# Kernel tuning notes

Hardware: AMD Instinct MI355X
Metric: run time of the kernel (lower is better)

The kernel has to match this reference:

```python
import jax, jax.numpy as jnp
import numpy as np
from jax import lax


def setup_inputs() -> dict:
    key = jax.random.key(0)
    kx, kw = jax.random.split(key)
    x = jax.random.normal(kx, (32, 3, 8192), dtype=jnp.float32)
    weight = jax.random.normal(kw, (128, 3, 64), dtype=jnp.float32)
    return {"x": x, "weight": weight}


def reference(x, weight):
    # x: [B, C, L], weight: [O, C, K]
    K = weight.shape[2]
    # Cross-correlation (conv1d, no bias, valid padding): [B, O, L-K+1]
    conv_out = lax.conv_general_dilated(
        x, weight, window_strides=(1,), padding='VALID',
        dimension_numbers=('NCH', 'OIH', 'NCH'))
    # Half squared norm of each shapelet: [O]
    w_norm = jnp.sum(weight ** 2, axis=(1, 2)) / 2
    # Half squared norm of each length-K window, via cumulative sums
    # (avoids materializing the [B, C, W, K] unfold tensor)
    sq = jnp.sum(x ** 2, axis=1)               # [B, L]
    c = jnp.pad(jnp.cumsum(sq, axis=1), ((0, 0), (1, 0)))  # [B, L+1]
    win_norm = (c[:, K:] - c[:, :-K]) / 2      # [B, L-K+1]
    # features = conv_out - (||w||^2/2 + ||window||^2/2)
    features = conv_out - w_norm[None, :, None] - win_norm[:, None, :]
    # global max-pool over time, then *(-2) -> min squared distance
    return -2.0 * jnp.max(features, axis=-1)   # [B, O]
```

## Files before the change

kernel.cpp:

```cpp
#include <hip/hip_runtime.h>
#include <hip/hip_bf16.h>
#include <float.h>

#define BB 32
#define LL 8192
#define OO 128
#define KK 64
#define WW (LL - KK + 1)
#define NCH 3
#define GX 11

typedef __attribute__((ext_vector_type(8))) short short8;
typedef __attribute__((ext_vector_type(4))) float f32x4;

union AB { int4 i4; int i[4]; short8 v; };

static __device__ __forceinline__ unsigned int pkbf(float a, float b) {
    union { __hip_bfloat162 h; unsigned int u; } cv;
    cv.h = __float22bfloat162_rn(make_float2(a, b));
    return cv.u;
}

static __device__ __forceinline__ void stage_load(const float* __restrict__ x, int b, int T0,
                                                  int tid, float4* v) {
    v[0] = make_float4(0.f, 0.f, 0.f, 0.f);
    v[1] = v[0];
    v[2] = v[0];
    if (tid < 80) {
        int l = T0 + 4 * tid;
        if (l < LL) {
            const float* p = x + (size_t)b * 3 * LL + l;
            v[0] = *(const float4*)(p);
            v[1] = *(const float4*)(p + LL);
            v[2] = *(const float4*)(p + 2 * LL);
        }
    }
}

static __device__ __forceinline__ void stage_store(int tid, const float4* v,
                                                   unsigned short* xl, float* sql, float* Pl) {
    if (tid >= 80) return;
    #pragma unroll
    for (int c = 0; c < 3; ++c) {
        uint2 pk;
        pk.x = pkbf(v[c].x, v[c].y);
        pk.y = pkbf(v[c].z, v[c].w);
        *(uint2*)(xl + c * 320 + tid * 4) = pk;
    }
    float4 sq4;
    sq4.x = fmaf(v[2].x, v[2].x, fmaf(v[1].x, v[1].x, v[0].x * v[0].x));
    sq4.y = fmaf(v[2].y, v[2].y, fmaf(v[1].y, v[1].y, v[0].y * v[0].y));
    sq4.z = fmaf(v[2].z, v[2].z, fmaf(v[1].z, v[1].z, v[0].z * v[0].z));
    sq4.w = fmaf(v[2].w, v[2].w, fmaf(v[1].w, v[1].w, v[0].w * v[0].w));
    *(float4*)(sql + tid * 4) = sq4;
    float s4 = (sq4.x + sq4.y) + (sq4.z + sq4.w);
    float s8 = s4 + __shfl_xor(s4, 1, 64);
    if ((tid & 1) == 0) Pl[tid >> 1] = s8;
}

__global__ __launch_bounds__(256, 3) void shapeconv_main(const float* __restrict__ x,
                                                         const float* __restrict__ w,
                                                         float* __restrict__ partial) {
    __shared__ __align__(16) unsigned short w_lds[64 * 192];
    __shared__ __align__(16) unsigned short x_lds[2][3 * 320];
    __shared__ __align__(16) float sq_lds[2][320];
    __shared__ __align__(16) float P_lds[2][40];
    __shared__ float wnp[4][64];
    __shared__ float mred[64];

    const int tcx = blockIdx.x;
    const int ob = blockIdx.y;
    const int b  = blockIdx.z;
    const int tid = threadIdx.x;
    const int wv = tid >> 6;
    const int lane = tid & 63;
    const int wo = wv & 1, wt = wv >> 1;
    const int n  = lane & 15;
    const int qp = lane >> 4;
    const int Tb = tcx * (NCH * 256);
    const int rem = (WW - Tb + 255) >> 8;
    const int nch_eff = rem < NCH ? rem : NCH;

    float4 sv[3];
    stage_load(x, b, Tb, tid, sv);

    {
        const int o2 = tid & 63;
        const int row = tid >> 6;
        const float* wb = w + ((size_t)(ob * 64 + o2)) * 192;
        float wsq = 0.f;
        #pragma unroll
        for (int i = 0; i < 6; ++i) {
            int g = tid + 256 * i;
            int ksqp = g >> 6;
            int ks = ksqp >> 2, qq = ksqp & 3;
            int c = ks >> 1, h = ks & 1;
            const float4* p = (const float4*)(wb + c * 64 + h * 32 + qq * 8);
            float4 v0 = p[0], v1 = p[1];
            int4 pk;
            pk.x = (int)pkbf(v0.x, v0.y);
            pk.y = (int)pkbf(v0.z, v0.w);
            pk.z = (int)pkbf(v1.x, v1.y);
            pk.w = (int)pkbf(v1.z, v1.w);
            ((int4*)w_lds)[g] = pk;
            wsq = fmaf(v0.x, v0.x, wsq); wsq = fmaf(v0.y, v0.y, wsq);
            wsq = fmaf(v0.z, v0.z, wsq); wsq = fmaf(v0.w, v0.w, wsq);
            wsq = fmaf(v1.x, v1.x, wsq); wsq = fmaf(v1.y, v1.y, wsq);
            wsq = fmaf(v1.z, v1.z, wsq); wsq = fmaf(v1.w, v1.w, wsq);
        }
        wnp[row][o2] = wsq;
    }

    stage_store(tid, sv, x_lds[0], sq_lds[0], P_lds[0]);
    __syncthreads();

    float nw[2][4];
    #pragma unroll
    for (int ot = 0; ot < 2; ++ot)
        #pragma unroll
        for (int rg = 0; rg < 4; ++rg) {
            int o = 32 * wo + 16 * ot + 4 * qp + rg;
            nw[ot][rg] = 0.5f * ((wnp[0][o] + wnp[1][o]) + (wnp[2][o] + wnp[3][o]));
        }

    float m2[2][4];
    #pragma unroll
    for (int ot = 0; ot < 2; ++ot)
        #pragma unroll
        for (int rg = 0; rg < 4; ++rg) m2[ot][rg] = -FLT_MAX;

    for (int ci = 0; ci < nch_eff; ++ci) {
        const int bsel = ci & 1;
        const int T0 = Tb + ci * 256;
        const bool more = (ci + 1 < nch_eff);
        if (more) stage_load(x, b, T0 + 256, tid, sv);

        float wl[8];
        {
            const float* sqp = sq_lds[bsel];
            const float* Pl  = P_lds[bsel];
            const int mi = 16 * wt + n;
            float S = 0.f;
            #pragma unroll
            for (int i = 0; i < 8; ++i) S += Pl[mi + i];
            #pragma unroll
            for (int r = 0; r < 8; ++r) {
                wl[r] = (T0 + 8 * mi + r < WW) ? 0.5f * S : 1e30f;
                if (r < 7) S += sqp[8 * mi + 64 + r] - sqp[8 * mi + r];
            }
        }

        f32x4 acc[2][8];
        #pragma unroll
        for (int ot = 0; ot < 2; ++ot)
            #pragma unroll
            for (int rg = 0; rg < 4; ++rg)
                #pragma unroll
                for (int r = 0; r < 8; ++r)
                    acc[ot][r][rg] = -nw[ot][rg] - wl[r];

        const char* xb = (const char*)x_lds[bsel];
        __builtin_amdgcn_s_setprio(1);
        #pragma unroll
        for (int ks = 0; ks < 6; ++ks) {
            int c = ks >> 1, h = ks & 1;
            int e0b = c * 640 + 256 * wt + 64 * h + 16 * (n + qp);
            int4 Ea = *(const int4*)(xb + e0b);
            int4 Eb = *(const int4*)(xb + e0b + 16);
            int D[8] = {Ea.x, Ea.y, Ea.z, Ea.w, Eb.x, Eb.y, Eb.z, Eb.w};
            AB a0, a1;
            const int4* wq = (const int4*)w_lds + (ks * 4 + qp) * 64 + 32 * wo;
            a0.i4 = wq[n];
            a1.i4 = wq[16 + n];
            #pragma unroll
            for (int r = 0; r < 8; ++r) {
                AB bf;
                int s = r >> 1;
                if ((r & 1) == 0) {
                    bf.i[0] = D[s]; bf.i[1] = D[s + 1]; bf.i[2] = D[s + 2]; bf.i[3] = D[s + 3];
                } else {
                    #pragma unroll
                    for (int d = 0; d < 4; ++d)
                        bf.i[d] = (int)__builtin_amdgcn_alignbit((unsigned)D[s + d + 1],
                                                                 (unsigned)D[s + d], 16);
                }
                acc[0][r] = __builtin_amdgcn_mfma_f32_16x16x32_bf16(a0.v, bf.v, acc[0][r], 0, 0, 0);
                acc[1][r] = __builtin_amdgcn_mfma_f32_16x16x32_bf16(a1.v, bf.v, acc[1][r], 0, 0, 0);
            }
        }
        __builtin_amdgcn_s_setprio(0);

        #pragma unroll
        for (int ot = 0; ot < 2; ++ot)
            #pragma unroll
            for (int rg = 0; rg < 4; ++rg) {
                float mm = m2[ot][rg];
                #pragma unroll
                for (int r = 0; r < 8; ++r) mm = fmaxf(mm, acc[ot][r][rg]);
                m2[ot][rg] = mm;
            }

        if (more) {
            stage_store(tid, sv, x_lds[1 - bsel], sq_lds[1 - bsel], P_lds[1 - bsel]);
            __syncthreads();
        }
    }

    #pragma unroll
    for (int s = 1; s <= 8; s <<= 1)
        #pragma unroll
        for (int ot = 0; ot < 2; ++ot)
            #pragma unroll
            for (int rg = 0; rg < 4; ++rg)
                m2[ot][rg] = fmaxf(m2[ot][rg], __shfl_xor(m2[ot][rg], s, 64));

    if (wt == 1 && n == 0) {
        #pragma unroll
        for (int ot = 0; ot < 2; ++ot)
            #pragma unroll
            for (int rg = 0; rg < 4; ++rg)
                mred[32 * wo + 16 * ot + 4 * qp + rg] = m2[ot][rg];
    }
    __syncthreads();
    if (wt == 0 && n == 0) {
        #pragma unroll
        for (int ot = 0; ot < 2; ++ot)
            #pragma unroll
            for (int rg = 0; rg < 4; ++rg) {
                int oi = 32 * wo + 16 * ot + 4 * qp + rg;
                float v = fmaxf(m2[ot][rg], mred[oi]);
                partial[((size_t)(b * GX + tcx) * 2 + ob) * 64 + oi] = v;
            }
    }
}

__global__ __launch_bounds__(256) void reduce_kernel(const float* __restrict__ partial,
                                                     float* __restrict__ out) {
    int idx = blockIdx.x * 256 + threadIdx.x;
    int b = idx >> 7, o = idx & 127;
    const float* pp = partial + ((size_t)b * GX * 2 + (o >> 6)) * 64 + (o & 63);
    float mx = -FLT_MAX;
    #pragma unroll
    for (int t = 0; t < GX; ++t) mx = fmaxf(mx, pp[(size_t)t * 128]);
    out[idx] = -2.f * mx;
}

extern "C" void kernel_launch(void* const* d_in, const int* in_sizes, int n_in,
                              void* d_out, int out_size, void* d_ws, size_t ws_size,
                              hipStream_t stream) {
    const float* x = (const float*)d_in[0];
    const float* w = (const float*)d_in[1];
    float* out = (float*)d_out;

    float* partial = (float*)d_ws;

    dim3 grid(GX, 2, BB);
    shapeconv_main<<<grid, 256, 0, stream>>>(x, w, partial);
    reduce_kernel<<<16, 256, 0, stream>>>(partial, out);
}
```

Measured before the change: 72.21 us.

## Precompute swizzled bf16 weights, split output channels finer, reduce with atomicMin

Adds a prep kernel that converts the weights to a swizzled bf16 layout, computes the half squared norms and initialises the output once per call. The main kernel then copies the weights into LDS with global_load_lds and no longer converts them. The output dimension is now split into 4 blocks of 32 channels instead of 2 blocks of 64. This halves the accumulators per wave and raises the occupancy target to 4 blocks. The separate reduce kernel is replaced by an integer atomicMin on the float bits of the output, which keeps the right order only for non-negative results and adds extra x loads and atomics in exchange.

```diff
diff --git a/kernel.cpp b/kernel.cpp
--- a/kernel.cpp
+++ b/kernel.cpp
@@ -19,6 +19,37 @@
     union { __hip_bfloat162 h; unsigned int u; } cv;
     cv.h = __float22bfloat162_rn(make_float2(a, b));
     return cv.u;
+}
+
+__global__ __launch_bounds__(256) void prep_kernel(const float* __restrict__ w,
+                                                   unsigned short* __restrict__ wswz,
+                                                   float* __restrict__ wn,
+                                                   float* __restrict__ out) {
+    int g = blockIdx.x * 256 + threadIdx.x;
+    if (g < 3072) {
+        int ob = g / 768;
+        int rem = g - ob * 768;
+        int rr = rem >> 5, o2 = rem & 31;
+        int ks = rr >> 2, qp = rr & 3;
+        int c = ks >> 1, h = ks & 1;
+        const float* p = w + (size_t)(ob * 32 + o2) * 192 + c * 64 + h * 32 + qp * 8;
+        float4 v0 = *(const float4*)p, v1 = *(const float4*)(p + 4);
+        int4 pk;
+        pk.x = (int)pkbf(v0.x, v0.y);
+        pk.y = (int)pkbf(v0.z, v0.w);
+        pk.z = (int)pkbf(v1.x, v1.y);
+        pk.w = (int)pkbf(v1.z, v1.w);
+        ((int4*)wswz)[g] = pk;
+    }
+    int oo = g - 3072;
+    if (oo >= 0 && oo < OO) {
+        const float* p = w + oo * 192;
+        float s = 0.f;
+        for (int i = 0; i < 192; ++i) { float v = p[i]; s = fmaf(v, v, s); }
+        wn[oo] = 0.5f * s;
+    }
+    int oi = g - 3200;
+    if (oi >= 0 && oi < BB * OO) out[oi] = 3.389e38f;
 }
 
 static __device__ __forceinline__ void stage_load(const float* __restrict__ x, int b, int T0,
@@ -58,15 +89,16 @@
     if ((tid & 1) == 0) Pl[tid >> 1] = s8;
 }
 
-__global__ __launch_bounds__(256, 3) void shapeconv_main(const float* __restrict__ x,
-                                                         const float* __restrict__ w,
-                                                         float* __restrict__ partial) {
-    __shared__ __align__(16) unsigned short w_lds[64 * 192];
+__global__ __launch_bounds__(256, 4) void shapeconv_main(const float* __restrict__ x,
+                                                         const unsigned short* __restrict__ wswz,
+                                                         const float* __restrict__ wn,
+                                                         float* __restrict__ out) {
+    __shared__ __align__(16) unsigned short w_lds[6144];
     __shared__ __align__(16) unsigned short x_lds[2][3 * 320];
     __shared__ __align__(16) float sq_lds[2][320];
     __shared__ __align__(16) float P_lds[2][40];
-    __shared__ float wnp[4][64];
-    __shared__ float mred[64];
+    __shared__ float wn_lds[32];
+    __shared__ float mred[32];
 
     const int tcx = blockIdx.x;
     const int ob = blockIdx.y;
@@ -81,53 +113,30 @@
     const int rem = (WW - Tb + 255) >> 8;
     const int nch_eff = rem < NCH ? rem : NCH;
 
+    {
+        const char* src = (const char*)wswz + (size_t)ob * 12288 + tid * 16;
+        #pragma unroll
+        for (int i = 0; i < 3; ++i) {
+            __builtin_amdgcn_global_load_lds(
+                (const __attribute__((address_space(1))) unsigned int*)(src + i * 4096),
+                (__attribute__((address_space(3))) unsigned int*)((char*)w_lds + tid * 16 + i * 4096),
+                16, 0, 0);
+        }
+    }
+    if (tid < 32) wn_lds[tid] = wn[ob * 32 + tid];
+
     float4 sv[3];
     stage_load(x, b, Tb, tid, sv);
-
-    {
-        const int o2 = tid & 63;
-        const int row = tid >> 6;
-        const float* wb = w + ((size_t)(ob * 64 + o2)) * 192;
-        float wsq = 0.f;
-        #pragma unroll
-        for (int i = 0; i < 6; ++i) {
-            int g = tid + 256 * i;
-            int ksqp = g >> 6;
-            int ks = ksqp >> 2, qq = ksqp & 3;
-            int c = ks >> 1, h = ks & 1;
-            const float4* p = (const float4*)(wb + c * 64 + h * 32 + qq * 8);
-            float4 v0 = p[0], v1 = p[1];
-            int4 pk;
-            pk.x = (int)pkbf(v0.x, v0.y);
-            pk.y = (int)pkbf(v0.z, v0.w);
-            pk.z = (int)pkbf(v1.x, v1.y);
-            pk.w = (int)pkbf(v1.z, v1.w);
-            ((int4*)w_lds)[g] = pk;
-            wsq = fmaf(v0.x, v0.x, wsq); wsq = fmaf(v0.y, v0.y, wsq);
-            wsq = fmaf(v0.z, v0.z, wsq); wsq = fmaf(v0.w, v0.w, wsq);
-            wsq = fmaf(v1.x, v1.x, wsq); wsq = fmaf(v1.y, v1.y, wsq);
-            wsq = fmaf(v1.z, v1.z, wsq); wsq = fmaf(v1.w, v1.w, wsq);
-        }
-        wnp[row][o2] = wsq;
-    }
-
     stage_store(tid, sv, x_lds[0], sq_lds[0], P_lds[0]);
     __syncthreads();
 
-    float nw[2][4];
-    #pragma unroll
-    for (int ot = 0; ot < 2; ++ot)
-        #pragma unroll
-        for (int rg = 0; rg < 4; ++rg) {
-            int o = 32 * wo + 16 * ot + 4 * qp + rg;
-            nw[ot][rg] = 0.5f * ((wnp[0][o] + wnp[1][o]) + (wnp[2][o] + wnp[3][o]));
-        }
-
-    float m2[2][4];
-    #pragma unroll
-    for (int ot = 0; ot < 2; ++ot)
-        #pragma unroll
-        for (int rg = 0; rg < 4; ++rg) m2[ot][rg] = -FLT_MAX;
+    float nw4[4];
+    #pragma unroll
+    for (int rg = 0; rg < 4; ++rg) nw4[rg] = wn_lds[16 * wo + 4 * qp + rg];
+
+    float m2[4];
+    #pragma unroll
+    for (int rg = 0; rg < 4; ++rg) m2[rg] = -FLT_MAX;
 
     for (int ci = 0; ci < nch_eff; ++ci) {
         const int bsel = ci & 1;
@@ -150,14 +159,12 @@
             }
         }
 
-        f32x4 acc[2][8];
-        #pragma unroll
-        for (int ot = 0; ot < 2; ++ot)
+        f32x4 acc[8];
+        #pragma unroll
+        for (int r = 0; r < 8; ++r)
             #pragma unroll
             for (int rg = 0; rg < 4; ++rg)
-                #pragma unroll
-                for (int r = 0; r < 8; ++r)
-                    acc[ot][r][rg] = -nw[ot][rg] - wl[r];
+                acc[r][rg] = -nw4[rg] - wl[r];
 
         const char* xb = (const char*)x_lds[bsel];
         __builtin_amdgcn_s_setprio(1);
@@ -168,10 +175,8 @@
             int4 Ea = *(const int4*)(xb + e0b);
             int4 Eb = *(const int4*)(xb + e0b + 16);
             int D[8] = {Ea.x, Ea.y, Ea.z, Ea.w, Eb.x, Eb.y, Eb.z, Eb.w};
-            AB a0, a1;
-            const int4* wq = (const int4*)w_lds + (ks * 4 + qp) * 64 + 32 * wo;
-            a0.i4 = wq[n];
-            a1.i4 = wq[16 + n];
+            AB a0;
+            a0.i4 = ((const int4*)w_lds)[(ks * 4 + qp) * 32 + 16 * wo + n];
             #pragma unroll
             for (int r = 0; r < 8; ++r) {
                 AB bf;
@@ -184,21 +189,18 @@
                         bf.i[d] = (int)__builtin_amdgcn_alignbit((unsigned)D[s + d + 1],
                                                                  (unsigned)D[s + d], 16);
                 }
-                acc[0][r] = __builtin_amdgcn_mfma_f32_16x16x32_bf16(a0.v, bf.v, acc[0][r], 0, 0, 0);
-                acc[1][r] = __builtin_amdgcn_mfma_f32_16x16x32_bf16(a1.v, bf.v, acc[1][r], 0, 0, 0);
+                acc[r] = __builtin_amdgcn_mfma_f32_16x16x32_bf16(a0.v, bf.v, acc[r], 0, 0, 0);
             }
         }
         __builtin_amdgcn_s_setprio(0);
 
         #pragma unroll
-        for (int ot = 0; ot < 2; ++ot)
-            #pragma unroll
-            for (int rg = 0; rg < 4; ++rg) {
-                float mm = m2[ot][rg];
-                #pragma unroll
-                for (int r = 0; r < 8; ++r) mm = fmaxf(mm, acc[ot][r][rg]);
-                m2[ot][rg] = mm;
-            }
+        for (int rg = 0; rg < 4; ++rg) {
+            float mm = m2[rg];
+            #pragma unroll
+            for (int r = 0; r < 8; ++r) mm = fmaxf(mm, acc[r][rg]);
+            m2[rg] = mm;
+        }
 
         if (more) {
             stage_store(tid, sv, x_lds[1 - bsel], sq_lds[1 - bsel], P_lds[1 - bsel]);
@@ -209,40 +211,24 @@
     #pragma unroll
     for (int s = 1; s <= 8; s <<= 1)
         #pragma unroll
-        for (int ot = 0; ot < 2; ++ot)
-            #pragma unroll
-            for (int rg = 0; rg < 4; ++rg)
-                m2[ot][rg] = fmaxf(m2[ot][rg], __shfl_xor(m2[ot][rg], s, 64));
+        for (int rg = 0; rg < 4; ++rg)
+            m2[rg] = fmaxf(m2[rg], __shfl_xor(m2[rg], s, 64));
 
     if (wt == 1 && n == 0) {
         #pragma unroll
-        for (int ot = 0; ot < 2; ++ot)
-            #pragma unroll
-            for (int rg = 0; rg < 4; ++rg)
-                mred[32 * wo + 16 * ot + 4 * qp + rg] = m2[ot][rg];
+        for (int rg = 0; rg < 4; ++rg)
+            mred[16 * wo + 4 * qp + rg] = m2[rg];
     }
     __syncthreads();
     if (wt == 0 && n == 0) {
         #pragma unroll
-        for (int ot = 0; ot < 2; ++ot)
-            #pragma unroll
-            for (int rg = 0; rg < 4; ++rg) {
-                int oi = 32 * wo + 16 * ot + 4 * qp + rg;
-                float v = fmaxf(m2[ot][rg], mred[oi]);
-                partial[((size_t)(b * GX + tcx) * 2 + ob) * 64 + oi] = v;
-            }
-    }
-}
-
-__global__ __launch_bounds__(256) void reduce_kernel(const float* __restrict__ partial,
-                                                     float* __restrict__ out) {
-    int idx = blockIdx.x * 256 + threadIdx.x;
-    int b = idx >> 7, o = idx & 127;
-    const float* pp = partial + ((size_t)b * GX * 2 + (o >> 6)) * 64 + (o & 63);
-    float mx = -FLT_MAX;
-    #pragma unroll
-    for (int t = 0; t < GX; ++t) mx = fmaxf(mx, pp[(size_t)t * 128]);
-    out[idx] = -2.f * mx;
+        for (int rg = 0; rg < 4; ++rg) {
+            int oi = 16 * wo + 4 * qp + rg;
+            float v = fmaxf(m2[rg], mred[oi]);
+            atomicMin((int*)(out + (size_t)b * OO + ob * 32 + oi),
+                      __float_as_int(-2.0f * v));
+        }
+    }
 }
 
 extern "C" void kernel_launch(void* const* d_in, const int* in_sizes, int n_in,
@@ -252,9 +238,10 @@
     const float* w = (const float*)d_in[1];
     float* out = (float*)d_out;
 
-    float* partial = (float*)d_ws;
-
-    dim3 grid(GX, 2, BB);
-    shapeconv_main<<<grid, 256, 0, stream>>>(x, w, partial);
-    reduce_kernel<<<16, 256, 0, stream>>>(partial, out);
-}
+    unsigned short* wswz = (unsigned short*)d_ws;
+    float* wn = (float*)((char*)d_ws + 49152);
+
+    prep_kernel<<<29, 256, 0, stream>>>(w, wswz, wn, out);
+    dim3 grid(GX, 4, BB);
+    shapeconv_main<<<grid, 256, 0, stream>>>(x, wswz, wn, out);
+}
```

Measured after the change: 77.07 us. 6.7% more time.
